# Kernel optimization log

Hardware: AMD Instinct MI355X
Metric: run time of the kernel (lower is better)

The kernel has to match this reference:

```python
import jax, jax.numpy as jnp
import numpy as np

B, S, D, H = 2, 2048, 1024, 16
DK = D // H


def setup_inputs() -> dict:
    key = jax.random.key(0)
    ks = jax.random.split(key, 12)
    sc = 0.02
    inp = {
        'query': jax.random.normal(ks[0], (B, S, D), jnp.float32),
        'key': jax.random.normal(ks[1], (B, S, D), jnp.float32),
        'value': jax.random.normal(ks[2], (B, S, D), jnp.float32),
        # causal mask: positions with mask==0 are disallowed (matches masked_fill(mask==0, -inf))
        'mask': jnp.broadcast_to(jnp.tril(jnp.ones((S, S), jnp.int32)), (B, S, S)),
        'Wq': jax.random.normal(ks[3], (D, D), jnp.float32) * sc,
        'bq': jax.random.normal(ks[4], (D,), jnp.float32) * sc,
        'Wk': jax.random.normal(ks[5], (D, D), jnp.float32) * sc,
        'bk': jax.random.normal(ks[6], (D,), jnp.float32) * sc,
        'Wv': jax.random.normal(ks[7], (D, D), jnp.float32) * sc,
        'bv': jax.random.normal(ks[8], (D,), jnp.float32) * sc,
        'Wo': jax.random.normal(ks[9], (D, D), jnp.float32) * sc,
        'bo': jax.random.normal(ks[10], (D,), jnp.float32) * sc,
    }
    return inp


def reference(query, key, value, mask, Wq, bq, Wk, bk, Wv, bv, Wo, bo):
    # Linear projections (torch Linear: x @ W.T + b), split heads -> [B,H,S,DK]
    def proj(x, W, b):
        return (x @ W.T + b).reshape(B, S, H, DK).transpose(0, 2, 1, 3)

    q = proj(query, Wq, bq)
    k = proj(key, Wk, bk)
    v = proj(value, Wv, bv)

    scores = jnp.einsum('bhqd,bhkd->bhqk', q, k) / jnp.sqrt(jnp.float32(DK))
    # mask unsqueezed over head dim: [B,1,S,S]
    scores = jnp.where(mask[:, None, :, :] == 0, -jnp.inf, scores)
    p = jax.nn.softmax(scores, axis=-1)
    x = jnp.einsum('bhqk,bhkd->bhqd', p, v)  # [B,H,S,DK]
    x = x.transpose(0, 2, 1, 3).reshape(B, S, D)
    return x @ Wo.T + bo
```

## Files before the change

### kernel.cpp

```cpp
#include <hip/hip_runtime.h>
#include <hip/hip_bf16.h>
#include <math.h>

#define BATCH 2
#define SEQ 2048
#define DMODEL 1024
#define NHEAD 16
#define DHEAD 64
#define MTOT (BATCH*SEQ)

typedef __attribute__((ext_vector_type(8))) short bf16x8;
typedef __attribute__((ext_vector_type(4))) short short4v;
typedef __attribute__((ext_vector_type(4))) float f32x4;

static __device__ inline short f2bs(float x) {
    __hip_bfloat16 b = __float2bfloat16(x);
    return *reinterpret_cast<short*>(&b);
}

static __device__ __forceinline__ void gload16(const void* g, void* l) {
    __builtin_amdgcn_global_load_lds(
        (const __attribute__((address_space(1))) unsigned int*)g,
        (__attribute__((address_space(3))) unsigned int*)l,
        16, 0, 0);
}

struct ConvArgs {
    const float* src[7];
    unsigned short* dst[7];
    int nblk[7];
};

__global__ __launch_bounds__(256)
void convert_bf16_kernel(ConvArgs a)
{
    int b = blockIdx.x;
    int r = 0;
    while (b >= a.nblk[r]) { b -= a.nblk[r]; ++r; }
    const float* s = a.src[r];
    unsigned short* d = a.dst[r];
    const int base = b * 2048 + threadIdx.x * 8;
    const float4 f0 = *reinterpret_cast<const float4*>(&s[base]);
    const float4 f1 = *reinterpret_cast<const float4*>(&s[base + 4]);
    bf16x8 o;
    o[0] = f2bs(f0.x); o[1] = f2bs(f0.y); o[2] = f2bs(f0.z); o[3] = f2bs(f0.w);
    o[4] = f2bs(f1.x); o[5] = f2bs(f1.y); o[6] = f2bs(f1.z); o[7] = f2bs(f1.w);
    *reinterpret_cast<bf16x8*>(&d[base]) = o;
}

template<int SPLIT>
static __device__ __forceinline__
void gemm_core(const short* __restrict__ Xg, const short* __restrict__ Wg,
               const float* __restrict__ bias, void* __restrict__ outp,
               float scale, int m0, int n0)
{
    __shared__ short Xs[2][128 * 64];
    __shared__ short Wt[2][128 * 64];

    const int t    = threadIdx.x;
    const int lane = t & 63;
    const int w    = t >> 6;
    const int wm   = w >> 1, wn = w & 1;
    const int m_   = lane & 15, g = lane >> 4;

    const int sr  = t >> 1;
    const int sc0 = (t & 1) * 4;

    f32x4 acc[4][4] = {};
    bf16x8 xr[4], wr[4];

    #pragma unroll
    for (int c = 0; c < 4; ++c) {
        xr[c] = *reinterpret_cast<const bf16x8*>(&Xg[(size_t)(m0 + sr) * DMODEL + (sc0 + c) * 8]);
        wr[c] = *reinterpret_cast<const bf16x8*>(&Wg[(size_t)(n0 + sr) * DMODEL + (sc0 + c) * 8]);
    }
    #pragma unroll
    for (int c = 0; c < 4; ++c) {
        const int byo = sr * 128 + (((sc0 + c) * 16) ^ ((sr & 7) << 4));
        *reinterpret_cast<bf16x8*>((char*)Xs[0] + byo) = xr[c];
        *reinterpret_cast<bf16x8*>((char*)Wt[0] + byo) = wr[c];
    }
    __syncthreads();

    for (int kt = 0; kt < DMODEL / 64; ++kt) {
        const int cur = kt & 1;
        const bool more = (kt < DMODEL / 64 - 1);

        if (more) {
            const int k0 = (kt + 1) * 64;
            #pragma unroll
            for (int c = 0; c < 4; ++c) {
                xr[c] = *reinterpret_cast<const bf16x8*>(&Xg[(size_t)(m0 + sr) * DMODEL + k0 + (sc0 + c) * 8]);
                wr[c] = *reinterpret_cast<const bf16x8*>(&Wg[(size_t)(n0 + sr) * DMODEL + k0 + (sc0 + c) * 8]);
            }
        }

        bf16x8 af[4][2], bfr[4][2];
        #pragma unroll
        for (int mt = 0; mt < 4; ++mt) {
            const int row = wm * 64 + mt * 16 + m_;
            #pragma unroll
            for (int kc = 0; kc < 2; ++kc)
                af[mt][kc] = *reinterpret_cast<const bf16x8*>(
                    (char*)Xs[cur] + row * 128 + ((kc * 64 + g * 16) ^ ((row & 7) << 4)));
        }
        #pragma unroll
        for (int nt = 0; nt < 4; ++nt) {
            const int row = wn * 64 + nt * 16 + m_;
            #pragma unroll
            for (int kc = 0; kc < 2; ++kc)
                bfr[nt][kc] = *reinterpret_cast<const bf16x8*>(
                    (char*)Wt[cur] + row * 128 + ((kc * 64 + g * 16) ^ ((row & 7) << 4)));
        }

        __builtin_amdgcn_s_setprio(1);
        #pragma unroll
        for (int mt = 0; mt < 4; ++mt)
            #pragma unroll
            for (int nt = 0; nt < 4; ++nt)
                #pragma unroll
                for (int kc = 0; kc < 2; ++kc)
                    acc[mt][nt] = __builtin_amdgcn_mfma_f32_16x16x32_bf16(
                        af[mt][kc], bfr[nt][kc], acc[mt][nt], 0, 0, 0);
        __builtin_amdgcn_s_setprio(0);

        if (more) {
            #pragma unroll
            for (int c = 0; c < 4; ++c) {
                const int byo = sr * 128 + (((sc0 + c) * 16) ^ ((sr & 7) << 4));
                *reinterpret_cast<bf16x8*>((char*)Xs[cur ^ 1] + byo) = xr[c];
                *reinterpret_cast<bf16x8*>((char*)Wt[cur ^ 1] + byo) = wr[c];
            }
        }
        __syncthreads();
    }

    float bv[4];
    #pragma unroll
    for (int nt = 0; nt < 4; ++nt) bv[nt] = bias[n0 + wn * 64 + nt * 16 + m_];

    #pragma unroll
    for (int mt = 0; mt < 4; ++mt) {
        #pragma unroll
        for (int r = 0; r < 4; ++r) {
            const int row = m0 + wm * 64 + mt * 16 + g * 4 + r;
            const int b = row >> 11;
            const int s = row & 2047;
            #pragma unroll
            for (int nt = 0; nt < 4; ++nt) {
                const int n = n0 + wn * 64 + nt * 16 + m_;
                const float c = (acc[mt][nt][r] + bv[nt]) * scale;
                if (SPLIT) {
                    const int h = n >> 6, dk = n & 63;
                    ((__hip_bfloat16*)outp)[(((size_t)(b * NHEAD + h)) * SEQ + s) * DHEAD + dk]
                        = __float2bfloat16(c);
                } else {
                    ((float*)outp)[(size_t)row * DMODEL + n] = c;
                }
            }
        }
    }
}

struct TrioArgs {
    const short* X[3];
    const short* W[3];
    const float* bias[3];
    __hip_bfloat16* out[3];
    float scale[3];
};

__global__ __launch_bounds__(256)
void gemm_qkv_kernel(TrioArgs a)
{
    const int which = blockIdx.x >> 8;
    const int tile  = blockIdx.x & 255;
    const int n0 = (tile & 7) * 128;
    const int m0 = (tile >> 3) * 128;
    gemm_core<1>(a.X[which], a.W[which], a.bias[which], a.out[which],
                 a.scale[which], m0, n0);
}

__global__ __launch_bounds__(256)
void gemm_out_kernel(const short* __restrict__ X, const short* __restrict__ W,
                     const float* __restrict__ bias, float* __restrict__ out)
{
    gemm_core<0>(X, W, bias, out, 1.0f, blockIdx.y * 128, blockIdx.x * 128);
}

__global__ __launch_bounds__(512, 4)
void attn_mfma_kernel(const __hip_bfloat16* __restrict__ Q,
                      const __hip_bfloat16* __restrict__ K,
                      const __hip_bfloat16* __restrict__ V,
                      __hip_bfloat16* __restrict__ ctx)
{
    __shared__ short Ks[2][64 * 64];
    __shared__ short Vts[2][64 * 64];
    __shared__ short Ps[8 * 16 * 72];

    const int t    = threadIdx.x;
    const int lane = t & 63;
    const int w    = t >> 6;
    const int wq   = w & 3;
    const int side = w >> 2;
    const int m    = lane & 15;
    const int g    = lane >> 4;

    const int bid = blockIdx.x;
    const int swz = (bid & 7) * 64 + (bid >> 3);
    const int bh  = swz >> 4;
    const int pr  = swz & 15;
    const int qtA = pr, qtB = 31 - pr;
    const int myqt = side ? qtB : qtA;
    const int q0   = myqt * 64;

    const __hip_bfloat16* Qb = Q + (size_t)bh * SEQ * DHEAD;
    const __hip_bfloat16* Kb = K + (size_t)bh * SEQ * DHEAD;
    const __hip_bfloat16* Vb = V + (size_t)bh * SEQ * DHEAD;

    const int sKrb = 16 * (w & 3);
    const int krl  = lane >> 3;
    const int kcs  = (lane & 7) ^ krl;
    const int vk   = t & 63;
    const int vd0  = ((t >> 6) & 3) * 16;

    bf16x8 vreg0, vreg1;
    auto stageK = [&](int k0s, int buf) {
        #pragma unroll
        for (int c2 = 0; c2 < 2; ++c2) {
            const int rb = sKrb + 8 * c2;
            gload16(Kb + (size_t)(k0s + rb + krl) * DHEAD + kcs * 8,
                    &Ks[buf][rb * 64]);
        }
    };
    auto loadV = [&](int k0s) {
        vreg0 = *reinterpret_cast<const bf16x8*>(&Vb[(size_t)(k0s + vk) * DHEAD + vd0]);
        vreg1 = *reinterpret_cast<const bf16x8*>(&Vb[(size_t)(k0s + vk) * DHEAD + vd0 + 8]);
    };
    auto writeV = [&](int buf) {
        #pragma unroll
        for (int j = 0; j < 8; ++j) {
            const int d = vd0 + j;
            *reinterpret_cast<short*>((char*)Vts[buf] +
                (((d * 128) + vk * 2) ^ ((d & 7) << 4))) = vreg0[j];
        }
        #pragma unroll
        for (int j = 0; j < 8; ++j) {
            const int d = vd0 + 8 + j;
            *reinterpret_cast<short*>((char*)Vts[buf] +
                (((d * 128) + vk * 2) ^ ((d & 7) << 4))) = vreg1[j];
        }
    };

    bf16x8 qf[2];
    #pragma unroll
    for (int c = 0; c < 2; ++c)
        qf[c] = *reinterpret_cast<const bf16x8*>(
            &Qb[(size_t)(q0 + 16 * wq + m) * DHEAD + c * 32 + 8 * g]);

    f32x4 o[4] = {};
    float mr = -INFINITY, lr = 0.0f;

    short* Pw = Ps + w * 16 * 72;

    if (t < 256) { stageK(0, 0); loadV(0); writeV(0); }
    __syncthreads();

    int cur = 0;
    for (int kt = 0; kt <= qtB; ++kt) {
        const bool more = (kt < qtB);
        if (t < 256 && more) {
            stageK((kt + 1) * 64, cur ^ 1);
            loadV((kt + 1) * 64);
        }

        if (kt <= myqt) {
            f32x4 s[4] = {};
            __builtin_amdgcn_s_setprio(1);
            #pragma unroll
            for (int ct = 0; ct < 4; ++ct) {
                const int krow = ct * 16 + m;
                #pragma unroll
                for (int c = 0; c < 2; ++c) {
                    const bf16x8 kf = *reinterpret_cast<const bf16x8*>((char*)Ks[cur] +
                        (((krow * 128) + c * 64 + 16 * g) ^ ((krow & 7) << 4)));
                    s[ct] = __builtin_amdgcn_mfma_f32_16x16x32_bf16(kf, qf[c], s[ct], 0, 0, 0);
                }
            }
            __builtin_amdgcn_s_setprio(0);

            if (kt == myqt) {
                const int qr = 16 * wq + m;
                #pragma unroll
                for (int ct = 0; ct < 4; ++ct)
                    #pragma unroll
                    for (int r = 0; r < 4; ++r)
                        if (ct * 16 + 4 * g + r > qr) s[ct][r] = -INFINITY;
            }

            float pmax = fmaxf(fmaxf(s[0][0], s[0][1]), fmaxf(s[0][2], s[0][3]));
            pmax = fmaxf(fmaxf(pmax, s[1][0]), s[1][1]);
            pmax = fmaxf(fmaxf(pmax, s[1][2]), s[1][3]);
            pmax = fmaxf(fmaxf(pmax, s[2][0]), s[2][1]);
            pmax = fmaxf(fmaxf(pmax, s[2][2]), s[2][3]);
            pmax = fmaxf(fmaxf(pmax, s[3][0]), s[3][1]);
            pmax = fmaxf(fmaxf(pmax, s[3][2]), s[3][3]);
            pmax = fmaxf(pmax, __shfl_xor(pmax, 16, 64));
            pmax = fmaxf(pmax, __shfl_xor(pmax, 32, 64));

            if (!__all(pmax <= mr + 8.0f)) {
                const float mnew = fmaxf(mr, pmax);
                const float scl  = __builtin_amdgcn_exp2f(mr - mnew);
                mr = mnew;
                lr *= scl;
                #pragma unroll
                for (int dt = 0; dt < 4; ++dt)
                    #pragma unroll
                    for (int r = 0; r < 4; ++r)
                        o[dt][r] *= scl;
            }

            float psum = 0.0f;
            #pragma unroll
            for (int ct = 0; ct < 4; ++ct) {
                #pragma unroll
                for (int r = 0; r < 4; ++r) {
                    s[ct][r] = __builtin_amdgcn_exp2f(s[ct][r] - mr);
                    psum += s[ct][r];
                }
            }
            psum += __shfl_xor(psum, 16, 64);
            psum += __shfl_xor(psum, 32, 64);
            lr += psum;

            #pragma unroll
            for (int ct = 0; ct < 4; ++ct) {
                short4v p4;
                p4[0] = f2bs(s[ct][0]); p4[1] = f2bs(s[ct][1]);
                p4[2] = f2bs(s[ct][2]); p4[3] = f2bs(s[ct][3]);
                *reinterpret_cast<short4v*>(&Pw[m * 72 + ct * 16 + 4 * g]) = p4;
            }

            bf16x8 pf[2];
            #pragma unroll
            for (int c = 0; c < 2; ++c)
                pf[c] = *reinterpret_cast<const bf16x8*>(&Pw[m * 72 + c * 32 + 8 * g]);

            __builtin_amdgcn_s_setprio(1);
            #pragma unroll
            for (int dt = 0; dt < 4; ++dt) {
                const int vrow = dt * 16 + m;
                #pragma unroll
                for (int c = 0; c < 2; ++c) {
                    const bf16x8 vf = *reinterpret_cast<const bf16x8*>((char*)Vts[cur] +
                        (((vrow * 128) + c * 64 + 16 * g) ^ ((vrow & 7) << 4)));
                    o[dt] = __builtin_amdgcn_mfma_f32_16x16x32_bf16(vf, pf[c], o[dt], 0, 0, 0);
                }
            }
            __builtin_amdgcn_s_setprio(0);
        }

        if (t < 256 && more) writeV(cur ^ 1);
        __syncthreads();
        cur ^= 1;
    }

    const int b = bh >> 4;
    const int h = bh & 15;
    const float inv = 1.0f / lr;
    const int row = q0 + 16 * wq + m;
    short* dst = (short*)&ctx[((size_t)(b * SEQ) + row) * DMODEL + h * DHEAD];
    #pragma unroll
    for (int dt = 0; dt < 4; ++dt) {
        short4v p4;
        p4[0] = f2bs(o[dt][0] * inv); p4[1] = f2bs(o[dt][1] * inv);
        p4[2] = f2bs(o[dt][2] * inv); p4[3] = f2bs(o[dt][3] * inv);
        *reinterpret_cast<short4v*>(dst + dt * 16 + 4 * g) = p4;
    }
}

extern "C" void kernel_launch(void* const* d_in, const int* in_sizes, int n_in,
                              void* d_out, int out_size, void* d_ws, size_t ws_size,
                              hipStream_t stream)
{
    const float* query = (const float*)d_in[0];
    const float* key   = (const float*)d_in[1];
    const float* value = (const float*)d_in[2];
    const float* Wq = (const float*)d_in[4];
    const float* bq = (const float*)d_in[5];
    const float* Wk = (const float*)d_in[6];
    const float* bk = (const float*)d_in[7];
    const float* Wv = (const float*)d_in[8];
    const float* bv = (const float*)d_in[9];
    const float* Wo = (const float*)d_in[10];
    const float* bo = (const float*)d_in[11];
    float* out = (float*)d_out;

    char* ws = (char*)d_ws;
    const size_t MB = 1024 * 1024;
    unsigned short* xq  = (unsigned short*)(ws + 0 * MB);
    unsigned short* xk  = (unsigned short*)(ws + 8 * MB);
    unsigned short* xv  = (unsigned short*)(ws + 16 * MB);
    unsigned short* wqb = (unsigned short*)(ws + 24 * MB);
    unsigned short* wkb = (unsigned short*)(ws + 26 * MB);
    unsigned short* wvb = (unsigned short*)(ws + 28 * MB);
    unsigned short* wob = (unsigned short*)(ws + 30 * MB);
    __hip_bfloat16* qb  = (__hip_bfloat16*)(ws + 32 * MB);
    __hip_bfloat16* kb  = (__hip_bfloat16*)(ws + 40 * MB);
    __hip_bfloat16* vb  = (__hip_bfloat16*)(ws + 48 * MB);
    __hip_bfloat16* ctx = (__hip_bfloat16*)(ws + 56 * MB);

    ConvArgs ca;
    ca.src[0] = query; ca.dst[0] = xq;  ca.nblk[0] = 2048;
    ca.src[1] = key;   ca.dst[1] = xk;  ca.nblk[1] = 2048;
    ca.src[2] = value; ca.dst[2] = xv;  ca.nblk[2] = 2048;
    ca.src[3] = Wq;    ca.dst[3] = wqb; ca.nblk[3] = 512;
    ca.src[4] = Wk;    ca.dst[4] = wkb; ca.nblk[4] = 512;
    ca.src[5] = Wv;    ca.dst[5] = wvb; ca.nblk[5] = 512;
    ca.src[6] = Wo;    ca.dst[6] = wob; ca.nblk[6] = 512;
    convert_bf16_kernel<<<dim3(8192), dim3(256), 0, stream>>>(ca);

    TrioArgs ta;
    ta.X[0] = (const short*)xq; ta.W[0] = (const short*)wqb; ta.bias[0] = bq;
    ta.out[0] = qb; ta.scale[0] = 0.125f * 1.44269504f;
    ta.X[1] = (const short*)xk; ta.W[1] = (const short*)wkb; ta.bias[1] = bk;
    ta.out[1] = kb; ta.scale[1] = 1.0f;
    ta.X[2] = (const short*)xv; ta.W[2] = (const short*)wvb; ta.bias[2] = bv;
    ta.out[2] = vb; ta.scale[2] = 1.0f;
    gemm_qkv_kernel<<<dim3(768), dim3(256), 0, stream>>>(ta);

    attn_mfma_kernel<<<dim3(512), dim3(512), 0, stream>>>(qb, kb, vb, ctx);

    gemm_out_kernel<<<dim3(8, 32), dim3(256), 0, stream>>>(
        (const short*)ctx, (const short*)wob, bo, out);
}
```

Baseline: 121.7 us.

## Single-buffer GEMM LDS tiles and swizzle block order for XCD locality

Shrinks the GEMM shared-memory tiles from double to single buffers, adding an extra barrier before each store so the tile is not overwritten while being read. This halves LDS use per block, which may allow more resident blocks. Block IDs for the QKV and output GEMMs are remapped so that consecutive blocks dispatched to the same XCD share input rows, aiming for better L2 reuse. The output GEMM launch becomes a 1-D grid. The extra barrier per k-step adds synchronization stalls.

```diff
diff --git a/kernel.cpp b/kernel.cpp
--- a/kernel.cpp
+++ b/kernel.cpp
@@ -54,8 +54,8 @@
                const float* __restrict__ bias, void* __restrict__ outp,
                float scale, int m0, int n0)
 {
-    __shared__ short Xs[2][128 * 64];
-    __shared__ short Wt[2][128 * 64];
+    __shared__ short Xs[128 * 64];
+    __shared__ short Wt[128 * 64];
 
     const int t    = threadIdx.x;
     const int lane = t & 63;
@@ -69,31 +69,29 @@
     f32x4 acc[4][4] = {};
     bf16x8 xr[4], wr[4];
 
-    #pragma unroll
-    for (int c = 0; c < 4; ++c) {
-        xr[c] = *reinterpret_cast<const bf16x8*>(&Xg[(size_t)(m0 + sr) * DMODEL + (sc0 + c) * 8]);
-        wr[c] = *reinterpret_cast<const bf16x8*>(&Wg[(size_t)(n0 + sr) * DMODEL + (sc0 + c) * 8]);
-    }
-    #pragma unroll
-    for (int c = 0; c < 4; ++c) {
-        const int byo = sr * 128 + (((sc0 + c) * 16) ^ ((sr & 7) << 4));
-        *reinterpret_cast<bf16x8*>((char*)Xs[0] + byo) = xr[c];
-        *reinterpret_cast<bf16x8*>((char*)Wt[0] + byo) = wr[c];
-    }
+    auto ldtile = [&](int k0) {
+        #pragma unroll
+        for (int c = 0; c < 4; ++c) {
+            xr[c] = *reinterpret_cast<const bf16x8*>(&Xg[(size_t)(m0 + sr) * DMODEL + k0 + (sc0 + c) * 8]);
+            wr[c] = *reinterpret_cast<const bf16x8*>(&Wg[(size_t)(n0 + sr) * DMODEL + k0 + (sc0 + c) * 8]);
+        }
+    };
+    auto sttile = [&]() {
+        #pragma unroll
+        for (int c = 0; c < 4; ++c) {
+            const int byo = sr * 128 + (((sc0 + c) * 16) ^ ((sr & 7) << 4));
+            *reinterpret_cast<bf16x8*>((char*)Xs + byo) = xr[c];
+            *reinterpret_cast<bf16x8*>((char*)Wt + byo) = wr[c];
+        }
+    };
+
+    ldtile(0);
+    sttile();
     __syncthreads();
 
     for (int kt = 0; kt < DMODEL / 64; ++kt) {
-        const int cur = kt & 1;
         const bool more = (kt < DMODEL / 64 - 1);
-
-        if (more) {
-            const int k0 = (kt + 1) * 64;
-            #pragma unroll
-            for (int c = 0; c < 4; ++c) {
-                xr[c] = *reinterpret_cast<const bf16x8*>(&Xg[(size_t)(m0 + sr) * DMODEL + k0 + (sc0 + c) * 8]);
-                wr[c] = *reinterpret_cast<const bf16x8*>(&Wg[(size_t)(n0 + sr) * DMODEL + k0 + (sc0 + c) * 8]);
-            }
-        }
+        if (more) ldtile((kt + 1) * 64);
 
         bf16x8 af[4][2], bfr[4][2];
         #pragma unroll
@@ -102,7 +100,7 @@
             #pragma unroll
             for (int kc = 0; kc < 2; ++kc)
                 af[mt][kc] = *reinterpret_cast<const bf16x8*>(
-                    (char*)Xs[cur] + row * 128 + ((kc * 64 + g * 16) ^ ((row & 7) << 4)));
+                    (char*)Xs + row * 128 + ((kc * 64 + g * 16) ^ ((row & 7) << 4)));
         }
         #pragma unroll
         for (int nt = 0; nt < 4; ++nt) {
@@ -110,7 +108,7 @@
             #pragma unroll
             for (int kc = 0; kc < 2; ++kc)
                 bfr[nt][kc] = *reinterpret_cast<const bf16x8*>(
-                    (char*)Wt[cur] + row * 128 + ((kc * 64 + g * 16) ^ ((row & 7) << 4)));
+                    (char*)Wt + row * 128 + ((kc * 64 + g * 16) ^ ((row & 7) << 4)));
         }
 
         __builtin_amdgcn_s_setprio(1);
@@ -124,14 +122,8 @@
                         af[mt][kc], bfr[nt][kc], acc[mt][nt], 0, 0, 0);
         __builtin_amdgcn_s_setprio(0);
 
-        if (more) {
-            #pragma unroll
-            for (int c = 0; c < 4; ++c) {
-                const int byo = sr * 128 + (((sc0 + c) * 16) ^ ((sr & 7) << 4));
-                *reinterpret_cast<bf16x8*>((char*)Xs[cur ^ 1] + byo) = xr[c];
-                *reinterpret_cast<bf16x8*>((char*)Wt[cur ^ 1] + byo) = wr[c];
-            }
-        }
+        __syncthreads();
+        if (more) sttile();
         __syncthreads();
     }
 
@@ -173,8 +165,10 @@
 __global__ __launch_bounds__(256)
 void gemm_qkv_kernel(TrioArgs a)
 {
-    const int which = blockIdx.x >> 8;
-    const int tile  = blockIdx.x & 255;
+    const int bid = blockIdx.x;
+    const int swz = (bid & 7) * 96 + (bid >> 3);
+    const int which = swz >> 8;
+    const int tile  = swz & 255;
     const int n0 = (tile & 7) * 128;
     const int m0 = (tile >> 3) * 128;
     gemm_core<1>(a.X[which], a.W[which], a.bias[which], a.out[which],
@@ -185,7 +179,11 @@
 void gemm_out_kernel(const short* __restrict__ X, const short* __restrict__ W,
                      const float* __restrict__ bias, float* __restrict__ out)
 {
-    gemm_core<0>(X, W, bias, out, 1.0f, blockIdx.y * 128, blockIdx.x * 128);
+    const int bid = blockIdx.x;
+    const int swz = (bid & 7) * 32 + (bid >> 3);
+    const int n0 = (swz & 7) * 128;
+    const int m0 = (swz >> 3) * 128;
+    gemm_core<0>(X, W, bias, out, 1.0f, m0, n0);
 }
 
 __global__ __launch_bounds__(512, 4)
@@ -431,6 +429,6 @@
 
     attn_mfma_kernel<<<dim3(512), dim3(512), 0, stream>>>(qb, kb, vb, ctx);
 
-    gemm_out_kernel<<<dim3(8, 32), dim3(256), 0, stream>>>(
+    gemm_out_kernel<<<dim3(256), dim3(256), 0, stream>>>(
         (const short*)ctx, (const short*)wob, bo, out);
 }
```

Result: faster. 116.4 us, median of 5 (-4.4%).
